# Optimization experiments

Hardware: AMD Instinct MI355X
Metric: run time of the kernel (lower is better)

The kernel has to match this reference:

```python
import jax, jax.numpy as jnp
import numpy as np

N_NODES = 50000
DROP_P = 0.25


def gcn_conv(x, edge_index, W, b, n_nodes):
    """PyG GCNConv: symmetric-normalized aggregation with self-loops.
    out = D^{-1/2} (A + I) D^{-1/2} (x @ W) + b
    """
    E = edge_index.shape[1]
    loops = jnp.arange(n_nodes, dtype=edge_index.dtype)
    src = jnp.concatenate([edge_index[0], loops])  # [E+N]
    dst = jnp.concatenate([edge_index[1], loops])  # [E+N]

    h = x @ W  # [N, out] dense GEMM

    ones = jnp.ones(E + n_nodes, dtype=x.dtype)
    deg = jax.ops.segment_sum(ones, dst, num_segments=n_nodes)  # [N]
    dinv = jnp.where(deg > 0, jax.lax.rsqrt(deg), 0.0)
    norm = dinv[src] * dinv[dst]  # [E+N]

    msgs = h[src] * norm[:, None]  # gather + scale, [E+N, out]
    out = jax.ops.segment_sum(msgs, dst, num_segments=n_nodes)  # scatter-add
    return out + b


def reference(x, edge_index, W1, b1, W2, b2):
    n = x.shape[0]
    h = gcn_conv(x, edge_index, W1, b1, n)
    h = jax.nn.elu(h)
    # F.dropout(p=0.25) defaults to training=True -> active dropout with
    # inverted scaling; deterministic mask from a fixed key.
    keep = jax.random.bernoulli(jax.random.key(42), 1.0 - DROP_P, h.shape)
    h = jnp.where(keep, h / (1.0 - DROP_P), 0.0).astype(h.dtype)
    out = gcn_conv(h, edge_index, W2, b2, n)
    return out


def setup_inputs() -> dict:
    key = jax.random.key(0)
    k1, k2, k3, k4 = jax.random.split(key, 4)
    C = 512
    E = 800000
    x = jax.random.normal(k1, (N_NODES, C), dtype=jnp.float32)
    edge_index = jax.random.randint(k2, (2, E), 0, N_NODES, dtype=jnp.int64)
    # Glorot-style scaled weights
    W1 = jax.random.normal(k3, (C, C // 2), dtype=jnp.float32) * (1.0 / np.sqrt(C))
    b1 = jnp.zeros((C // 2,), dtype=jnp.float32)
    W2 = jax.random.normal(k4, (C // 2, 1), dtype=jnp.float32) * (1.0 / np.sqrt(C // 2))
    b2 = jnp.zeros((1,), dtype=jnp.float32)
    return {"x": x, "edge_index": edge_index, "W1": W1, "b1": b1, "W2": W2, "b2": b2}
```

## Files before the change

kernel.cpp:

```cpp
#include <hip/hip_runtime.h>
#include <stdint.h>


typedef float floatx4 __attribute__((ext_vector_type(4)));
typedef _Float16 f16;
typedef _Float16 f16x8 __attribute__((ext_vector_type(8)));

union F16x8 {
  f16x8 v;
  f16 e[8];
  uint4 q;
};

__device__ __forceinline__ void tf_round(uint32_t& x0, uint32_t& x1, int r) {
  x0 += x1;
  x1 = (x1 << r) | (x1 >> (32 - r));
  x1 ^= x0;
}

__device__ __forceinline__ void threefry_0_42(uint32_t c0, uint32_t c1,
                                              uint32_t& o0, uint32_t& o1) {
  const uint32_t ks0 = 0u;
  const uint32_t ks1 = 42u;
  const uint32_t ks2 = 0x1BD11BDAu ^ 0u ^ 42u;
  uint32_t x0 = c0 + ks0;
  uint32_t x1 = c1 + ks1;
  tf_round(x0, x1, 13); tf_round(x0, x1, 15); tf_round(x0, x1, 26); tf_round(x0, x1, 6);
  x0 += ks1; x1 += ks2 + 1u;
  tf_round(x0, x1, 17); tf_round(x0, x1, 29); tf_round(x0, x1, 16); tf_round(x0, x1, 24);
  x0 += ks2; x1 += ks0 + 2u;
  tf_round(x0, x1, 13); tf_round(x0, x1, 15); tf_round(x0, x1, 26); tf_round(x0, x1, 6);
  x0 += ks0; x1 += ks1 + 3u;
  tf_round(x0, x1, 17); tf_round(x0, x1, 29); tf_round(x0, x1, 16); tf_round(x0, x1, 24);
  x0 += ks1; x1 += ks2 + 4u;
  tf_round(x0, x1, 13); tf_round(x0, x1, 15); tf_round(x0, x1, 26); tf_round(x0, x1, 6);
  x0 += ks2; x1 += ks0 + 5u;
  o0 = x0; o1 = x1;
}

__device__ __forceinline__ unsigned char mask_byte(uint32_t b) {
  uint32_t jb = b << 3;
  uint32_t m = 0;
#pragma unroll
  for (int i = 0; i < 8; ++i) {
    uint32_t r0, r1;
    threefry_0_42(0u, jb + (uint32_t)i, r0, r1);
    uint32_t bits = r0 ^ r1;
    m |= (bits < 0xC0000000u ? 1u : 0u) << i;
  }
  return (unsigned char)m;
}

__global__ void k_deg(const int* __restrict__ dst, int E, int* __restrict__ deg,
                      unsigned char* __restrict__ maskb, int nb0) {
  int t = blockIdx.x * blockDim.x + threadIdx.x;
  if (t < E) atomicAdd(&deg[dst[t]], 1);
  if (t < nb0) maskb[t] = mask_byte((uint32_t)t);
}

__global__ __launch_bounds__(256) void k_scan1(const int* __restrict__ deg,
                                               int* __restrict__ excl,
                                               int* __restrict__ sums,
                                               float* __restrict__ dinv, int N) {
  __shared__ int sm[256];
  int tid = threadIdx.x;
  int i = blockIdx.x * 256 + tid;
  int v = (i < N) ? deg[i] : 0;
  if (i < N) dinv[i] = 1.0f / sqrtf((float)(v + 1));
  sm[tid] = v;
  __syncthreads();
#pragma unroll
  for (int off = 1; off < 256; off <<= 1) {
    int t = (tid >= off) ? sm[tid - off] : 0;
    __syncthreads();
    sm[tid] += t;
    __syncthreads();
  }
  if (i < N) excl[i] = sm[tid] - v;
  if (tid == 255) sums[blockIdx.x] = sm[255];
}

__global__ __launch_bounds__(1024) void k_scan2(int* __restrict__ sums, int nb) {
  __shared__ int sm[1024];
  int tid = threadIdx.x;
  int v = (tid < nb) ? sums[tid] : 0;
  sm[tid] = v;
  __syncthreads();
#pragma unroll
  for (int off = 1; off < 1024; off <<= 1) {
    int t = (tid >= off) ? sm[tid - off] : 0;
    __syncthreads();
    sm[tid] += t;
    __syncthreads();
  }
  if (tid < nb) sums[tid] = sm[tid] - v;
}

__global__ void k_scan3(int* __restrict__ rowptr, int* __restrict__ cursor,
                        const int* __restrict__ sums, int N, int E) {
  int i = blockIdx.x * blockDim.x + threadIdx.x;
  if (i < N) {
    int r = rowptr[i] + sums[i >> 8];
    rowptr[i] = r;
    cursor[i] = r;
  }
  if (i == 0) rowptr[N] = E;
}

__global__ void k_bucket(const int* __restrict__ src, const int* __restrict__ dst,
                         int* __restrict__ cursor, int* __restrict__ csr_src, int E,
                         unsigned char* __restrict__ maskb, int nb0, int nb1) {
  int t = blockIdx.x * blockDim.x + threadIdx.x;
  if (t < E) {
    int pos = atomicAdd(&cursor[dst[t]], 1);
    csr_src[pos] = src[t];
  }
  if (t < nb1) maskb[nb0 + t] = mask_byte((uint32_t)(nb0 + t));
}

__global__ void k_prep_w1t(const float* __restrict__ W1,
                           f16* __restrict__ Bpk) {
  int t = blockIdx.x * blockDim.x + threadIdx.x;
  if (t >= 512 * 256) return;
  int k = t >> 8, n = t & 255;
  int ks = k >> 5, quad = (k >> 3) & 3, j = k & 7;
  int nt = n >> 4, lane = quad * 16 + (n & 15);
  size_t e = ((size_t)(ks * 16 + nt)) * 64 + lane;
  Bpk[e * 8 + j] = (f16)W1[t];
}

__global__ __launch_bounds__(256) void k_gemm_mfma(
    const float* __restrict__ A,
    const uint4* __restrict__ Bpk,
    const float* __restrict__ dinv,
    f16* __restrict__ C,
    int M) {
  __shared__ f16 As[2][64 * 40];
  const int tid = threadIdx.x;
  const int cg = tid >> 6;
  const int lane = tid & 63;
  const int quad = lane >> 4;
  const int l16 = lane & 15;
  const int m0 = blockIdx.x * 64;

  const int srow = tid >> 2;
  const int scq = tid & 3;
  int grow = m0 + srow;
  if (grow >= M) grow = M - 1;
  const float* gsp = A + (size_t)grow * 512 + scq * 8;
  f16* lwp = &As[0][srow * 40 + scq * 8];
  const int lstride = 64 * 40;

  auto cvt8 = [](float4 a, float4 b) {
    F16x8 r;
    r.e[0] = (f16)a.x; r.e[1] = (f16)a.y; r.e[2] = (f16)a.z; r.e[3] = (f16)a.w;
    r.e[4] = (f16)b.x; r.e[5] = (f16)b.y; r.e[6] = (f16)b.z; r.e[7] = (f16)b.w;
    return r;
  };

  {
    float4 s0 = *(const float4*)(gsp);
    float4 s1 = *(const float4*)(gsp + 4);
    *(uint4*)lwp = cvt8(s0, s1).q;
  }
  __syncthreads();

  floatx4 acc[4][4];
#pragma unroll
  for (int fr = 0; fr < 4; ++fr)
#pragma unroll
    for (int t = 0; t < 4; ++t) acc[fr][t] = (floatx4){0.f, 0.f, 0.f, 0.f};

  const uint4* bp0 = Bpk + lane + (size_t)(cg * 4) * 64;

  for (int ks = 0; ks < 16; ++ks) {
    const int cur = ks & 1;
    const int nxt = cur ^ 1;

    float4 p0, p1;
    if (ks < 15) {
      p0 = *(const float4*)(gsp + (ks + 1) * 32);
      p1 = *(const float4*)(gsp + (ks + 1) * 32 + 4);
    }

    const uint4* bp = bp0 + (size_t)ks * 1024;
    F16x8 bfrag[4];
#pragma unroll
    for (int t = 0; t < 4; ++t) bfrag[t].q = bp[t * 64];

#pragma unroll
    for (int fr = 0; fr < 4; ++fr) {
      F16x8 af;
      af.q = *(const uint4*)&As[cur][(fr * 16 + l16) * 40 + quad * 8];
#pragma unroll
      for (int t = 0; t < 4; ++t) {
        acc[fr][t] = __builtin_amdgcn_mfma_f32_16x16x32_f16(af.v, bfrag[t].v, acc[fr][t], 0, 0, 0);
      }
    }

    if (ks < 15) {
      *(uint4*)(lwp + nxt * lstride) = cvt8(p0, p1).q;
    }
    __syncthreads();
  }

#pragma unroll
  for (int fr = 0; fr < 4; ++fr)
#pragma unroll
    for (int r = 0; r < 4; ++r) {
      int gm = m0 + fr * 16 + quad * 4 + r;
      if (gm < M) {
        float dv = dinv[gm];
#pragma unroll
        for (int t = 0; t < 4; ++t) {
          const int col = (cg * 4 + t) * 16 + l16;
          C[(size_t)gm * 256 + col] = (f16)(dv * acc[fr][t][r]);
        }
      }
    }
}

__global__ __launch_bounds__(256) void k_gather_fused(
    const int* __restrict__ rowptr, const int* __restrict__ csr_src,
    const float* __restrict__ dinv, const f16* __restrict__ hs,
    const float* __restrict__ b1, const float* __restrict__ W2,
    const unsigned char* __restrict__ maskb,
    float* __restrict__ zs, int N) {
  int wave = (blockIdx.x * blockDim.x + threadIdx.x) >> 6;
  int lane = threadIdx.x & 63;
  int half = lane >> 5;
  int l = lane & 31;
  int d = wave * 2 + half;
  bool valid = d < N;
  if (!valid) d = N - 1;
  float dd = dinv[d];
  int beg = rowptr[d], end = rowptr[d + 1];
  int f0 = l << 3;

  F16x8 accu;
  accu.q = *(const uint4*)(hs + ((size_t)d << 8) + f0);
  f16x8 accv = accu.v;

  int e = beg;
  {
    int pe = beg + ((4 - (beg & 3)) & 3);
    if (pe > end) pe = end;
    for (; e < pe; ++e) {
      F16x8 a;
      a.q = *(const uint4*)(hs + ((size_t)csr_src[e] << 8) + f0);
      accv = accv + a.v;
    }
  }
  for (; e + 3 < end; e += 4) {
    int4 s4 = *(const int4*)(csr_src + e);
    F16x8 a, b, c, dq;
    a.q  = *(const uint4*)(hs + ((size_t)s4.x << 8) + f0);
    b.q  = *(const uint4*)(hs + ((size_t)s4.y << 8) + f0);
    c.q  = *(const uint4*)(hs + ((size_t)s4.z << 8) + f0);
    dq.q = *(const uint4*)(hs + ((size_t)s4.w << 8) + f0);
    f16x8 t0 = a.v + b.v;
    f16x8 t1 = c.v + dq.v;
    accv = accv + (t0 + t1);
  }
  for (; e < end; ++e) {
    F16x8 a;
    a.q = *(const uint4*)(hs + ((size_t)csr_src[e] << 8) + f0);
    accv = accv + a.v;
  }
  accu.v = accv;

  float4 bb0 = *(const float4*)(b1 + f0);
  float4 bb1 = *(const float4*)(b1 + f0 + 4);
  float4 w0  = *(const float4*)(W2 + f0);
  float4 w1  = *(const float4*)(W2 + f0 + 4);
  const float* bbp[8] = {&bb0.x, &bb0.y, &bb0.z, &bb0.w, &bb1.x, &bb1.y, &bb1.z, &bb1.w};
  const float* wp[8]  = {&w0.x, &w0.y, &w0.z, &w0.w, &w1.x, &w1.y, &w1.z, &w1.w};

  uint32_t mb = maskb[(size_t)d * 32 + l];

  float sum = 0.f;
#pragma unroll
  for (int i = 0; i < 8; ++i) {
    float va = dd * (float)accu.e[i] + *bbp[i];
    float ea = va > 0.f ? va : (__expf(va) - 1.0f);
    float ha = ((mb >> i) & 1u) ? (ea * (1.0f / 0.75f)) : 0.f;
    sum += ha * *wp[i];
  }
#pragma unroll
  for (int off = 16; off > 0; off >>= 1) sum += __shfl_down(sum, off, 32);
  if (l == 0 && valid) zs[d] = dd * sum;
}

__global__ __launch_bounds__(256) void k_gather2(
    const int* __restrict__ rowptr, const int* __restrict__ csr_src,
    const float* __restrict__ dinv, const float* __restrict__ zs,
    const float* __restrict__ b2, float* __restrict__ out, int N) {
  int wave = (blockIdx.x * blockDim.x + threadIdx.x) >> 6;
  int lane = threadIdx.x & 63;
  int sub = lane >> 4;
  int l = lane & 15;
  int d = wave * 4 + sub;
  bool valid = d < N;
  if (!valid) d = N - 1;
  float dd = dinv[d];
  int beg = rowptr[d], end = rowptr[d + 1];

  float acc = 0.f;
  for (int e = beg + l; e < end; e += 16) {
    acc += zs[csr_src[e]];
  }
#pragma unroll
  for (int off = 8; off > 0; off >>= 1) acc += __shfl_down(acc, off, 16);
  if (l == 0 && valid) out[d] = b2[0] + dd * (zs[d] + acc);
}

extern "C" void kernel_launch(void* const* d_in, const int* in_sizes, int n_in,
                              void* d_out, int out_size, void* d_ws, size_t ws_size,
                              hipStream_t stream) {
  const float* x  = (const float*)d_in[0];
  const int*   ei = (const int*)d_in[1];
  const float* W1 = (const float*)d_in[2];
  const float* b1 = (const float*)d_in[3];
  const float* W2 = (const float*)d_in[4];
  const float* b2 = (const float*)d_in[5];
  float* out = (float*)d_out;

  const int E = in_sizes[1] / 2;
  const int N = in_sizes[0] / 512;
  const int* src = ei;
  const int* dst = ei + E;

  char* ws = (char*)d_ws;
  size_t off = 0;
  auto alloc = [&](size_t bytes) -> void* {
    void* p = ws + off;
    off += (bytes + 255) & ~(size_t)255;
    return p;
  };
  int*   deg     = (int*)  alloc((size_t)N * 4);
  int*   rowptr  = (int*)  alloc((size_t)(N + 1) * 4);
  int*   cursor  = (int*)  alloc((size_t)N * 4);
  int*   csr_src = (int*)  alloc((size_t)E * 4);
  int*   sums    = (int*)  alloc(1024 * 4);
  float* dinv    = (float*)alloc((size_t)N * 4);
  f16*   hs      = (f16*)  alloc((size_t)N * 256 * 2);
  float* zs      = (float*)alloc((size_t)N * 4);
  f16*   Bpk     = (f16*)  alloc(512 * 256 * 2);
  unsigned char* maskb = (unsigned char*)alloc((size_t)N * 32);

  const int nb = (N + 255) / 256;

  const int nbytes = N * 32;
  const int nb0 = nbytes >> 1;
  const int nb1 = nbytes - nb0;
  const int tdeg = (E > nb0) ? E : nb0;
  const int tbkt = (E > nb1) ? E : nb1;

  hipMemsetAsync(deg, 0, (size_t)N * 4, stream);
  k_prep_w1t<<<(512 * 256 + 255) / 256, 256, 0, stream>>>(W1, Bpk);
  k_deg<<<(tdeg + 255) / 256, 256, 0, stream>>>(dst, E, deg, maskb, nb0);
  k_scan1<<<nb, 256, 0, stream>>>(deg, rowptr, sums, dinv, N);
  k_scan2<<<1, 1024, 0, stream>>>(sums, nb);
  k_scan3<<<(N + 255) / 256, 256, 0, stream>>>(rowptr, cursor, sums, N, E);
  k_bucket<<<(tbkt + 255) / 256, 256, 0, stream>>>(src, dst, cursor, csr_src, E,
                                                   maskb, nb0, nb1);

  k_gemm_mfma<<<(N + 63) / 64, 256, 0, stream>>>(x, (const uint4*)Bpk, dinv, hs, N);

  const int nwaves1 = (N + 1) / 2;
  k_gather_fused<<<(nwaves1 * 64 + 255) / 256, 256, 0, stream>>>(rowptr, csr_src, dinv, hs,
                                                                 b1, W2, maskb, zs, N);
  const int nwaves2 = (N + 3) / 4;
  k_gather2<<<(nwaves2 * 64 + 255) / 256, 256, 0, stream>>>(rowptr, csr_src, dinv, zs, b2, out, N);
}
```

Baseline: 345.6 us.

## Load GEMM A fragments directly into registers, dropping LDS staging and barriers

The MFMA GEMM no longer stages the fp32 A tile through shared memory with per-step barriers. Each wavefront now loads its own A fragment rows from global memory, converts them to fp16 in registers, and double-buffers both A and B fragments in registers with a fully unrolled K loop. This removes LDS writes/reads and __syncthreads. In exchange, all four wavefronts redundantly fetch the same A rows from global/cache, and more registers are used.

New measurement: 386.7 us. 1.12x slower.

```diff
diff --git a/kernel.cpp b/kernel.cpp
--- a/kernel.cpp
+++ b/kernel.cpp
@@ -135,7 +135,6 @@
     const float* __restrict__ dinv,
     f16* __restrict__ C,
     int M) {
-  __shared__ f16 As[2][64 * 40];
   const int tid = threadIdx.x;
   const int cg = tid >> 6;
   const int lane = tid & 63;
@@ -143,13 +142,14 @@
   const int l16 = lane & 15;
   const int m0 = blockIdx.x * 64;
 
-  const int srow = tid >> 2;
-  const int scq = tid & 3;
-  int grow = m0 + srow;
-  if (grow >= M) grow = M - 1;
-  const float* gsp = A + (size_t)grow * 512 + scq * 8;
-  f16* lwp = &As[0][srow * 40 + scq * 8];
-  const int lstride = 64 * 40;
+  const float* ap[4];
+#pragma unroll
+  for (int fr = 0; fr < 4; ++fr) {
+    int r = m0 + fr * 16 + l16;
+    if (r >= M) r = M - 1;
+    ap[fr] = A + (size_t)r * 512 + quad * 8;
+  }
+  const uint4* bp0 = Bpk + lane + (size_t)(cg * 4) * 64;
 
   auto cvt8 = [](float4 a, float4 b) {
     F16x8 r;
@@ -158,50 +158,49 @@
     return r;
   };
 
-  {
-    float4 s0 = *(const float4*)(gsp);
-    float4 s1 = *(const float4*)(gsp + 4);
-    *(uint4*)lwp = cvt8(s0, s1).q;
-  }
-  __syncthreads();
-
   floatx4 acc[4][4];
 #pragma unroll
   for (int fr = 0; fr < 4; ++fr)
 #pragma unroll
     for (int t = 0; t < 4; ++t) acc[fr][t] = (floatx4){0.f, 0.f, 0.f, 0.f};
 
-  const uint4* bp0 = Bpk + lane + (size_t)(cg * 4) * 64;
-
+  float4 pa[2][4][2];
+  uint4 pb[2][4];
+
+#pragma unroll
+  for (int fr = 0; fr < 4; ++fr) {
+    pa[0][fr][0] = *(const float4*)(ap[fr]);
+    pa[0][fr][1] = *(const float4*)(ap[fr] + 4);
+  }
+#pragma unroll
+  for (int t = 0; t < 4; ++t) pb[0][t] = bp0[t * 64];
+
+#pragma unroll
   for (int ks = 0; ks < 16; ++ks) {
     const int cur = ks & 1;
     const int nxt = cur ^ 1;
 
-    float4 p0, p1;
     if (ks < 15) {
-      p0 = *(const float4*)(gsp + (ks + 1) * 32);
-      p1 = *(const float4*)(gsp + (ks + 1) * 32 + 4);
+#pragma unroll
+      for (int fr = 0; fr < 4; ++fr) {
+        pa[nxt][fr][0] = *(const float4*)(ap[fr] + (ks + 1) * 32);
+        pa[nxt][fr][1] = *(const float4*)(ap[fr] + (ks + 1) * 32 + 4);
+      }
+      const uint4* bp = bp0 + (size_t)(ks + 1) * 1024;
+#pragma unroll
+      for (int t = 0; t < 4; ++t) pb[nxt][t] = bp[t * 64];
     }
 
-    const uint4* bp = bp0 + (size_t)ks * 1024;
-    F16x8 bfrag[4];
-#pragma unroll
-    for (int t = 0; t < 4; ++t) bfrag[t].q = bp[t * 64];
-
 #pragma unroll
     for (int fr = 0; fr < 4; ++fr) {
-      F16x8 af;
-      af.q = *(const uint4*)&As[cur][(fr * 16 + l16) * 40 + quad * 8];
+      F16x8 af = cvt8(pa[cur][fr][0], pa[cur][fr][1]);
 #pragma unroll
       for (int t = 0; t < 4; ++t) {
-        acc[fr][t] = __builtin_amdgcn_mfma_f32_16x16x32_f16(af.v, bfrag[t].v, acc[fr][t], 0, 0, 0);
+        F16x8 bf;
+        bf.q = pb[cur][t];
+        acc[fr][t] = __builtin_amdgcn_mfma_f32_16x16x32_f16(af.v, bf.v, acc[fr][t], 0, 0, 0);
       }
     }
-
-    if (ks < 15) {
-      *(uint4*)(lwp + nxt * lstride) = cvt8(p0, p1).q;
-    }
-    __syncthreads();
   }
 
 #pragma unroll
```

## Stage full 64x512 A tile in XOR-swizzled LDS and drop per-k barriers

Applied to the files above, without the earlier changes.

The GEMM kernel now loads the whole 64-row by 512-column fp32 A tile, converted to fp16, into a 64 KB shared buffer up front. It then runs the 16 k-steps fully unrolled with no barrier between them. Row offsets are XOR-swizzled so the LDS reads are free of bank conflicts even without padding. This removes 15 __syncthreads and the double-buffer handoff. The cost is 64 KB of LDS per block, which lowers occupancy, and the loss of overlap between global loads and MFMA work.

New measurement: 338.2 us. 2.1% less time.

```diff
diff --git a/kernel.cpp b/kernel.cpp
--- a/kernel.cpp
+++ b/kernel.cpp
@@ -135,7 +135,7 @@
     const float* __restrict__ dinv,
     f16* __restrict__ C,
     int M) {
-  __shared__ f16 As[2][64 * 40];
+  __shared__ char As[64 * 1024];
   const int tid = threadIdx.x;
   const int cg = tid >> 6;
   const int lane = tid & 63;
@@ -143,14 +143,6 @@
   const int l16 = lane & 15;
   const int m0 = blockIdx.x * 64;
 
-  const int srow = tid >> 2;
-  const int scq = tid & 3;
-  int grow = m0 + srow;
-  if (grow >= M) grow = M - 1;
-  const float* gsp = A + (size_t)grow * 512 + scq * 8;
-  f16* lwp = &As[0][srow * 40 + scq * 8];
-  const int lstride = 64 * 40;
-
   auto cvt8 = [](float4 a, float4 b) {
     F16x8 r;
     r.e[0] = (f16)a.x; r.e[1] = (f16)a.y; r.e[2] = (f16)a.z; r.e[3] = (f16)a.w;
@@ -159,9 +151,19 @@
   };
 
   {
-    float4 s0 = *(const float4*)(gsp);
-    float4 s1 = *(const float4*)(gsp + 4);
-    *(uint4*)lwp = cvt8(s0, s1).q;
+    const int srow = tid >> 2;
+    const int scq = tid & 3;
+    int grow = m0 + srow;
+    if (grow >= M) grow = M - 1;
+    const float* gsp = A + (size_t)grow * 512 + scq * 8;
+    char* lbase = As + srow * 1024;
+    const int swz = (srow & 7) << 4;
+#pragma unroll
+    for (int ks = 0; ks < 16; ++ks) {
+      float4 s0 = *(const float4*)(gsp + ks * 32);
+      float4 s1 = *(const float4*)(gsp + ks * 32 + 4);
+      *(uint4*)(lbase + ((scq * 16 + ks * 64) ^ swz)) = cvt8(s0, s1).q;
+    }
   }
   __syncthreads();
 
@@ -172,36 +174,25 @@
     for (int t = 0; t < 4; ++t) acc[fr][t] = (floatx4){0.f, 0.f, 0.f, 0.f};
 
   const uint4* bp0 = Bpk + lane + (size_t)(cg * 4) * 64;
-
+  const int swzr = (l16 & 7) << 4;
+
+#pragma unroll
   for (int ks = 0; ks < 16; ++ks) {
-    const int cur = ks & 1;
-    const int nxt = cur ^ 1;
-
-    float4 p0, p1;
-    if (ks < 15) {
-      p0 = *(const float4*)(gsp + (ks + 1) * 32);
-      p1 = *(const float4*)(gsp + (ks + 1) * 32 + 4);
-    }
-
     const uint4* bp = bp0 + (size_t)ks * 1024;
-    F16x8 bfrag[4];
-#pragma unroll
-    for (int t = 0; t < 4; ++t) bfrag[t].q = bp[t * 64];
+    F16x8 bf[4];
+#pragma unroll
+    for (int t = 0; t < 4; ++t) bf[t].q = bp[t * 64];
 
 #pragma unroll
     for (int fr = 0; fr < 4; ++fr) {
+      const int row = fr * 16 + l16;
       F16x8 af;
-      af.q = *(const uint4*)&As[cur][(fr * 16 + l16) * 40 + quad * 8];
+      af.q = *(const uint4*)(As + row * 1024 + ((quad * 16 + ks * 64) ^ swzr));
 #pragma unroll
       for (int t = 0; t < 4; ++t) {
-        acc[fr][t] = __builtin_amdgcn_mfma_f32_16x16x32_f16(af.v, bfrag[t].v, acc[fr][t], 0, 0, 0);
+        acc[fr][t] = __builtin_amdgcn_mfma_f32_16x16x32_f16(af.v, bf[t].v, acc[fr][t], 0, 0, 0);
       }
     }
-
-    if (ks < 15) {
-      *(uint4*)(lwp + nxt * lstride) = cvt8(p0, p1).q;
-    }
-    __syncthreads();
   }
 
 #pragma unroll
```
